# Optimization experiments

Hardware: AMD Instinct MI355X
Metric: run time of the kernel (lower is better)

## Reference

```python
import jax, jax.numpy as jnp
import numpy as np

B, K, VOC, D = 1024, 5, 32000, 128


def setup_inputs() -> dict:
    key = jax.random.key(0)
    k1, k2, k3, k4, k5 = jax.random.split(key, 5)
    return {
        "vi": jax.random.normal(k1, (B, VOC), dtype=jnp.float32),
        "vo": jax.random.normal(k2, (B, VOC), dtype=jnp.float32),
        "neg_samples": jax.random.normal(k3, (B, K, VOC), dtype=jnp.float32),
        "V": jax.random.normal(k4, (VOC, D), dtype=jnp.float32),
        "U": jax.random.normal(k5, (VOC, D), dtype=jnp.float32),
    }


def reference(vi, vo, neg_samples, V, U):
    # one-hot-style matmul embedding lookups
    vi_embed = vi @ V                                  # [B, D]
    vo_embed = vo @ U                                  # [B, D]
    # positive term: logsigmoid(<vi_embed, vo_embed>)
    left = jax.nn.log_sigmoid(jnp.sum(vi_embed * vo_embed, axis=1, keepdims=True))  # [B, 1]
    # negative samples: [B, K, D] then batched dot with vi_embed
    neg_embed = jnp.einsum("bkv,vd->bkd", neg_samples, U)   # [B, K, D]
    batch_mul = jnp.einsum("bkd,bd->bk", neg_embed, vi_embed)  # [B, K]
    right = jnp.sum(jax.nn.log_sigmoid(-batch_mul), axis=1, keepdims=True)  # [B, 1]
    return jnp.mean(-(left + right))
```

## Files before the change

### kernel.cpp

```cpp
#include <hip/hip_runtime.h>
#include <hip/hip_bf16.h>

#define B_SZ 1024
#define KNEG 5
#define VOC 32000
#define DIM 128

typedef __bf16 bf16x8 __attribute__((ext_vector_type(8)));
typedef float f32x4 __attribute__((ext_vector_type(4)));


__device__ __forceinline__ float logsig(float x) {
    return fminf(x, 0.0f) - log1pf(expf(-fabsf(x)));
}

__global__ __launch_bounds__(256) void k0_convert(
    const float* __restrict__ V, const float* __restrict__ U,
    __bf16* __restrict__ Vt, __bf16* __restrict__ Ub) {
    __shared__ float tile[32][33];
    int bid = blockIdx.x;
    int vt = bid >> 2;
    int dt = bid & 3;
    int v0 = vt * 32, d0 = dt * 32;
    int t = threadIdx.x;
    int lr = t >> 5;
    int lc = t & 31;
#pragma unroll
    for (int i = 0; i < 4; ++i) {
        int r = lr + i * 8;
        size_t idx = (size_t)(v0 + r) * DIM + d0 + lc;
        tile[r][lc] = V[idx];
        Ub[idx] = (__bf16)U[idx];
    }
    __syncthreads();
#pragma unroll
    for (int i = 0; i < 4; ++i) {
        int r = lr + i * 8;
        Vt[(size_t)(d0 + r) * VOC + v0 + lc] = (__bf16)tile[lc][r];
    }
}

__global__ __launch_bounds__(256) void k1_viembed(
    const float* __restrict__ vi, const __bf16* __restrict__ Vt,
    float* __restrict__ partial) {
    int mt = blockIdx.x;
    int sp = blockIdx.y;
    int wave = threadIdx.x >> 6;
    int lane = threadIdx.x & 63;
    int n16 = lane & 15;
    int q = lane >> 4;
    int b0 = mt * 32;

    f32x4 acc[2][8];
#pragma unroll
    for (int rt = 0; rt < 2; ++rt)
#pragma unroll
        for (int ct = 0; ct < 8; ++ct)
            acc[rt][ct] = (f32x4){0.f, 0.f, 0.f, 0.f};

    int v_base = sp * 4000;
    for (int s = wave; s < 125; s += 4) {
        int kk = v_base + s * 32 + q * 8;
        bf16x8 afrag[2];
#pragma unroll
        for (int rt = 0; rt < 2; ++rt) {
            int b = b0 + rt * 16 + n16;
            const float4* p = (const float4*)(vi + (size_t)b * VOC + kk);
            float4 x0 = p[0];
            float4 x1 = p[1];
            bf16x8 a;
            a[0] = (__bf16)x0.x; a[1] = (__bf16)x0.y;
            a[2] = (__bf16)x0.z; a[3] = (__bf16)x0.w;
            a[4] = (__bf16)x1.x; a[5] = (__bf16)x1.y;
            a[6] = (__bf16)x1.z; a[7] = (__bf16)x1.w;
            afrag[rt] = a;
        }
#pragma unroll
        for (int ct = 0; ct < 8; ++ct) {
            int d = ct * 16 + n16;
            bf16x8 bfrag = *(const bf16x8*)(Vt + (size_t)d * VOC + kk);
#pragma unroll
            for (int rt = 0; rt < 2; ++rt)
                acc[rt][ct] = __builtin_amdgcn_mfma_f32_16x16x32_bf16(
                    afrag[rt], bfrag, acc[rt][ct], 0, 0, 0);
        }
    }

    __shared__ float red[4][32][128];
#pragma unroll
    for (int rt = 0; rt < 2; ++rt)
#pragma unroll
        for (int ct = 0; ct < 8; ++ct)
#pragma unroll
            for (int r = 0; r < 4; ++r)
                red[wave][rt * 16 + q * 4 + r][ct * 16 + n16] = acc[rt][ct][r];
    __syncthreads();
    int t = threadIdx.x;
#pragma unroll
    for (int i = 0; i < 16; ++i) {
        int idx = t + i * 256;
        int bl = idx >> 7, dd = idx & 127;
        float s = red[0][bl][dd] + red[1][bl][dd] + red[2][bl][dd] + red[3][bl][dd];
        partial[((size_t)sp * B_SZ + b0 + bl) * DIM + dd] = s;
    }
}

__global__ __launch_bounds__(256) void k2_reduce(
    const float* __restrict__ partial, __bf16* __restrict__ vie) {
    int idx = blockIdx.x * 256 + threadIdx.x;
    float s = 0.f;
#pragma unroll
    for (int sp = 0; sp < 8; ++sp) s += partial[(size_t)sp * (B_SZ * DIM) + idx];
    vie[idx] = (__bf16)s;
}

__global__ __launch_bounds__(256) void k3_fused(
    const __bf16* __restrict__ vie, const float* __restrict__ vo,
    const float* __restrict__ neg, const __bf16* __restrict__ Ub,
    float* __restrict__ pos_dot, float* __restrict__ neg_dot) {
    __shared__ float W[32 * 256];
    int bt = blockIdx.x;
    int vc = blockIdx.y;
    int t = threadIdx.x;
    int wave = t >> 6, lane = t & 63, n16 = lane & 15, q = lane >> 4;
    int b0 = bt * 32;

    bf16x8 afrag[2][4];
#pragma unroll
    for (int rt = 0; rt < 2; ++rt) {
        int b = b0 + rt * 16 + n16;
#pragma unroll
        for (int ks = 0; ks < 4; ++ks)
            afrag[rt][ks] = *(const bf16x8*)(vie + (size_t)b * DIM + ks * 32 + q * 8);
    }

    int rowB = t >> 3;
    int lcol = t & 7;
    float acc[6] = {0.f, 0.f, 0.f, 0.f, 0.f, 0.f};

    int vbase = vc * 1280;
    const float* vop = vo + (size_t)(b0 + rowB) * VOC + vbase + lcol * 4;
    const float* negp[KNEG];
#pragma unroll
    for (int k = 0; k < KNEG; ++k)
        negp[k] = neg + ((size_t)(b0 + rowB) * KNEG + k) * VOC + vbase + lcol * 4;

    for (int c = 0; c < 5; ++c) {
        int vchunk = vbase + c * 256;
#pragma unroll
        for (int j = 0; j < 4; ++j) {
            int tt = wave * 4 + j;
            int v0 = vchunk + tt * 16;
            f32x4 w0 = (f32x4){0.f, 0.f, 0.f, 0.f};
            f32x4 w1 = (f32x4){0.f, 0.f, 0.f, 0.f};
#pragma unroll
            for (int ks = 0; ks < 4; ++ks) {
                bf16x8 bfrag = *(const bf16x8*)(Ub + (size_t)(v0 + n16) * DIM + ks * 32 + q * 8);
                w0 = __builtin_amdgcn_mfma_f32_16x16x32_bf16(afrag[0][ks], bfrag, w0, 0, 0, 0);
                w1 = __builtin_amdgcn_mfma_f32_16x16x32_bf16(afrag[1][ks], bfrag, w1, 0, 0, 0);
            }
            int col = tt * 16 + n16;
#pragma unroll
            for (int r = 0; r < 4; ++r) {
                W[(q * 4 + r) * 256 + col] = w0[r];
                W[(16 + q * 4 + r) * 256 + col] = w1[r];
            }
        }
        __syncthreads();
        const float* vpc = vop + c * 256;
#pragma unroll
        for (int i = 0; i < 8; ++i) {
            float4 wv = *(const float4*)&W[rowB * 256 + lcol * 4 + i * 32];
            float4 x = *(const float4*)(vpc + i * 32);
            acc[0] += x.x * wv.x + x.y * wv.y + x.z * wv.z + x.w * wv.w;
#pragma unroll
            for (int k = 0; k < KNEG; ++k) {
                float4 y = *(const float4*)(negp[k] + c * 256 + i * 32);
                acc[1 + k] += y.x * wv.x + y.y * wv.y + y.z * wv.z + y.w * wv.w;
            }
        }
        __syncthreads();
    }

#pragma unroll
    for (int j = 0; j < 6; ++j) {
        float s = acc[j];
        s += __shfl_xor(s, 1, 8);
        s += __shfl_xor(s, 2, 8);
        s += __shfl_xor(s, 4, 8);
        if (lcol == 0) {
            int b = b0 + rowB;
            if (j == 0) atomicAdd(&pos_dot[b], s);
            else atomicAdd(&neg_dot[b * KNEG + (j - 1)], s);
        }
    }
}

__global__ __launch_bounds__(256) void k4_final(
    const float* __restrict__ pos_dot, const float* __restrict__ neg_dot,
    float* __restrict__ out) {
    __shared__ float wsum[4];
    int t = threadIdx.x;
    float s = 0.f;
    for (int b = t; b < B_SZ; b += 256) {
        float left = logsig(pos_dot[b]);
        float right = 0.f;
#pragma unroll
        for (int k = 0; k < KNEG; ++k) right += logsig(-neg_dot[b * KNEG + k]);
        s += -(left + right);
    }
#pragma unroll
    for (int m = 32; m >= 1; m >>= 1) s += __shfl_xor(s, m, 64);
    if ((t & 63) == 0) wsum[t >> 6] = s;
    __syncthreads();
    if (t == 0) out[0] = (wsum[0] + wsum[1] + wsum[2] + wsum[3]) * (1.0f / B_SZ);
}

extern "C" void kernel_launch(void* const* d_in, const int* in_sizes, int n_in,
                              void* d_out, int out_size, void* d_ws, size_t ws_size,
                              hipStream_t stream) {
    const float* vi  = (const float*)d_in[0];
    const float* vo  = (const float*)d_in[1];
    const float* neg = (const float*)d_in[2];
    const float* V   = (const float*)d_in[3];
    const float* U   = (const float*)d_in[4];

    char* ws = (char*)d_ws;
    __bf16* Ub      = (__bf16*)(ws);
    __bf16* Vt      = (__bf16*)(ws + 8192000);
    float*  partial = (float*) (ws + 16384000);
    __bf16* vie     = (__bf16*)(ws + 20578304);
    float*  pos_dot = (float*) (ws + 20840448);
    float*  neg_dot = (float*) (ws + 20844544);
    float*  out     = (float*)d_out;

    hipMemsetAsync(ws + 20840448, 0, 4096 + 20480, stream);

    k0_convert<<<4000, 256, 0, stream>>>(V, U, Vt, Ub);
    k1_viembed<<<dim3(32, 8), 256, 0, stream>>>(vi, Vt, partial);
    k2_reduce<<<512, 256, 0, stream>>>(partial, vie);
    k3_fused<<<dim3(32, 25), 256, 0, stream>>>(vie, vo, neg, Ub, pos_dot, neg_dot);
    k4_final<<<1, 256, 0, stream>>>(pos_dot, neg_dot, out);
}
```

Baseline: 1.117 ms.

## Increase split-K parallelism in vi embedding and negative-sample kernels

The vi@V kernel moves from 256 blocks, each reducing over 4000 vocab entries with an in-block LDS cross-wave reduction, to 800 blocks where each wave owns 16 batch rows over a 640-wide vocab slice and writes its partial directly. The reduction kernel now sums 50 partials. The fused vo/neg kernel drops its 5-chunk loop so each block handles a single 256-wide slice, giving 4000 blocks instead of 800. The aim is more concurrent blocks to saturate memory bandwidth on the large streaming reads, at the cost of a much larger partial buffer, more atomics and repeated vie fragment loads.

```diff
diff --git a/kernel.cpp b/kernel.cpp
--- a/kernel.cpp
+++ b/kernel.cpp
@@ -5,6 +5,9 @@
 #define KNEG 5
 #define VOC 32000
 #define DIM 128
+#define NSPLIT 50
+#define VSLICE 640
+#define NS (VSLICE / 32)
 
 typedef __bf16 bf16x8 __attribute__((ext_vector_type(8)));
 typedef float f32x4 __attribute__((ext_vector_type(4)));
@@ -49,60 +52,36 @@
     int lane = threadIdx.x & 63;
     int n16 = lane & 15;
     int q = lane >> 4;
-    int b0 = mt * 32;
-
-    f32x4 acc[2][8];
-#pragma unroll
-    for (int rt = 0; rt < 2; ++rt)
-#pragma unroll
-        for (int ct = 0; ct < 8; ++ct)
-            acc[rt][ct] = (f32x4){0.f, 0.f, 0.f, 0.f};
-
-    int v_base = sp * 4000;
-    for (int s = wave; s < 125; s += 4) {
+    int brow = mt * 64 + wave * 16;
+
+    f32x4 acc[8];
+#pragma unroll
+    for (int ct = 0; ct < 8; ++ct) acc[ct] = (f32x4){0.f, 0.f, 0.f, 0.f};
+
+    int v_base = sp * VSLICE;
+    const float* arow = vi + (size_t)(brow + n16) * VOC + v_base + q * 8;
+#pragma unroll 2
+    for (int s = 0; s < NS; ++s) {
         int kk = v_base + s * 32 + q * 8;
-        bf16x8 afrag[2];
-#pragma unroll
-        for (int rt = 0; rt < 2; ++rt) {
-            int b = b0 + rt * 16 + n16;
-            const float4* p = (const float4*)(vi + (size_t)b * VOC + kk);
-            float4 x0 = p[0];
-            float4 x1 = p[1];
-            bf16x8 a;
-            a[0] = (__bf16)x0.x; a[1] = (__bf16)x0.y;
-            a[2] = (__bf16)x0.z; a[3] = (__bf16)x0.w;
-            a[4] = (__bf16)x1.x; a[5] = (__bf16)x1.y;
-            a[6] = (__bf16)x1.z; a[7] = (__bf16)x1.w;
-            afrag[rt] = a;
-        }
+        float4 x0 = *(const float4*)(arow + s * 32);
+        float4 x1 = *(const float4*)(arow + s * 32 + 4);
+        bf16x8 a;
+        a[0] = (__bf16)x0.x; a[1] = (__bf16)x0.y;
+        a[2] = (__bf16)x0.z; a[3] = (__bf16)x0.w;
+        a[4] = (__bf16)x1.x; a[5] = (__bf16)x1.y;
+        a[6] = (__bf16)x1.z; a[7] = (__bf16)x1.w;
 #pragma unroll
         for (int ct = 0; ct < 8; ++ct) {
-            int d = ct * 16 + n16;
-            bf16x8 bfrag = *(const bf16x8*)(Vt + (size_t)d * VOC + kk);
-#pragma unroll
-            for (int rt = 0; rt < 2; ++rt)
-                acc[rt][ct] = __builtin_amdgcn_mfma_f32_16x16x32_bf16(
-                    afrag[rt], bfrag, acc[rt][ct], 0, 0, 0);
-        }
-    }
-
-    __shared__ float red[4][32][128];
-#pragma unroll
-    for (int rt = 0; rt < 2; ++rt)
-#pragma unroll
-        for (int ct = 0; ct < 8; ++ct)
-#pragma unroll
-            for (int r = 0; r < 4; ++r)
-                red[wave][rt * 16 + q * 4 + r][ct * 16 + n16] = acc[rt][ct][r];
-    __syncthreads();
-    int t = threadIdx.x;
-#pragma unroll
-    for (int i = 0; i < 16; ++i) {
-        int idx = t + i * 256;
-        int bl = idx >> 7, dd = idx & 127;
-        float s = red[0][bl][dd] + red[1][bl][dd] + red[2][bl][dd] + red[3][bl][dd];
-        partial[((size_t)sp * B_SZ + b0 + bl) * DIM + dd] = s;
-    }
+            bf16x8 bfrag = *(const bf16x8*)(Vt + (size_t)(ct * 16 + n16) * VOC + kk);
+            acc[ct] = __builtin_amdgcn_mfma_f32_16x16x32_bf16(a, bfrag, acc[ct], 0, 0, 0);
+        }
+    }
+    float* pb = partial + ((size_t)sp * B_SZ + brow) * DIM;
+#pragma unroll
+    for (int ct = 0; ct < 8; ++ct)
+#pragma unroll
+        for (int r = 0; r < 4; ++r)
+            pb[(size_t)(q * 4 + r) * DIM + ct * 16 + n16] = acc[ct][r];
 }
 
 __global__ __launch_bounds__(256) void k2_reduce(
@@ -110,7 +89,7 @@
     int idx = blockIdx.x * 256 + threadIdx.x;
     float s = 0.f;
 #pragma unroll
-    for (int sp = 0; sp < 8; ++sp) s += partial[(size_t)sp * (B_SZ * DIM) + idx];
+    for (int sp = 0; sp < NSPLIT; ++sp) s += partial[(size_t)sp * (B_SZ * DIM) + idx];
     vie[idx] = (__bf16)s;
 }
 
@@ -124,6 +103,7 @@
     int t = threadIdx.x;
     int wave = t >> 6, lane = t & 63, n16 = lane & 15, q = lane >> 4;
     int b0 = bt * 32;
+    int vbase = vc * 256;
 
     bf16x8 afrag[2][4];
 #pragma unroll
@@ -133,53 +113,48 @@
         for (int ks = 0; ks < 4; ++ks)
             afrag[rt][ks] = *(const bf16x8*)(vie + (size_t)b * DIM + ks * 32 + q * 8);
     }
+
+#pragma unroll
+    for (int j = 0; j < 4; ++j) {
+        int tt = wave * 4 + j;
+        int v0 = vbase + tt * 16;
+        f32x4 w0 = (f32x4){0.f, 0.f, 0.f, 0.f};
+        f32x4 w1 = (f32x4){0.f, 0.f, 0.f, 0.f};
+#pragma unroll
+        for (int ks = 0; ks < 4; ++ks) {
+            bf16x8 bfrag = *(const bf16x8*)(Ub + (size_t)(v0 + n16) * DIM + ks * 32 + q * 8);
+            w0 = __builtin_amdgcn_mfma_f32_16x16x32_bf16(afrag[0][ks], bfrag, w0, 0, 0, 0);
+            w1 = __builtin_amdgcn_mfma_f32_16x16x32_bf16(afrag[1][ks], bfrag, w1, 0, 0, 0);
+        }
+        int col = tt * 16 + n16;
+#pragma unroll
+        for (int r = 0; r < 4; ++r) {
+            W[(q * 4 + r) * 256 + col] = w0[r];
+            W[(16 + q * 4 + r) * 256 + col] = w1[r];
+        }
+    }
+    __syncthreads();
 
     int rowB = t >> 3;
     int lcol = t & 7;
     float acc[6] = {0.f, 0.f, 0.f, 0.f, 0.f, 0.f};
 
-    int vbase = vc * 1280;
     const float* vop = vo + (size_t)(b0 + rowB) * VOC + vbase + lcol * 4;
     const float* negp[KNEG];
 #pragma unroll
     for (int k = 0; k < KNEG; ++k)
         negp[k] = neg + ((size_t)(b0 + rowB) * KNEG + k) * VOC + vbase + lcol * 4;
 
-    for (int c = 0; c < 5; ++c) {
-        int vchunk = vbase + c * 256;
-#pragma unroll
-        for (int j = 0; j < 4; ++j) {
-            int tt = wave * 4 + j;
-            int v0 = vchunk + tt * 16;
-            f32x4 w0 = (f32x4){0.f, 0.f, 0.f, 0.f};
-            f32x4 w1 = (f32x4){0.f, 0.f, 0.f, 0.f};
-#pragma unroll
-            for (int ks = 0; ks < 4; ++ks) {
-                bf16x8 bfrag = *(const bf16x8*)(Ub + (size_t)(v0 + n16) * DIM + ks * 32 + q * 8);
-                w0 = __builtin_amdgcn_mfma_f32_16x16x32_bf16(afrag[0][ks], bfrag, w0, 0, 0, 0);
-                w1 = __builtin_amdgcn_mfma_f32_16x16x32_bf16(afrag[1][ks], bfrag, w1, 0, 0, 0);
-            }
-            int col = tt * 16 + n16;
-#pragma unroll
-            for (int r = 0; r < 4; ++r) {
-                W[(q * 4 + r) * 256 + col] = w0[r];
-                W[(16 + q * 4 + r) * 256 + col] = w1[r];
-            }
-        }
-        __syncthreads();
-        const float* vpc = vop + c * 256;
-#pragma unroll
-        for (int i = 0; i < 8; ++i) {
-            float4 wv = *(const float4*)&W[rowB * 256 + lcol * 4 + i * 32];
-            float4 x = *(const float4*)(vpc + i * 32);
-            acc[0] += x.x * wv.x + x.y * wv.y + x.z * wv.z + x.w * wv.w;
-#pragma unroll
-            for (int k = 0; k < KNEG; ++k) {
-                float4 y = *(const float4*)(negp[k] + c * 256 + i * 32);
-                acc[1 + k] += y.x * wv.x + y.y * wv.y + y.z * wv.z + y.w * wv.w;
-            }
-        }
-        __syncthreads();
+#pragma unroll
+    for (int i = 0; i < 8; ++i) {
+        float4 wv = *(const float4*)&W[rowB * 256 + lcol * 4 + i * 32];
+        float4 x = *(const float4*)(vop + i * 32);
+        acc[0] += x.x * wv.x + x.y * wv.y + x.z * wv.z + x.w * wv.w;
+#pragma unroll
+        for (int k = 0; k < KNEG; ++k) {
+            float4 y = *(const float4*)(negp[k] + i * 32);
+            acc[1 + k] += y.x * wv.x + y.y * wv.y + y.z * wv.z + y.w * wv.w;
+        }
     }
 
 #pragma unroll
@@ -229,16 +204,16 @@
     __bf16* Ub      = (__bf16*)(ws);
     __bf16* Vt      = (__bf16*)(ws + 8192000);
     float*  partial = (float*) (ws + 16384000);
-    __bf16* vie     = (__bf16*)(ws + 20578304);
-    float*  pos_dot = (float*) (ws + 20840448);
-    float*  neg_dot = (float*) (ws + 20844544);
+    __bf16* vie     = (__bf16*)(ws + 42598400);
+    float*  pos_dot = (float*) (ws + 42860544);
+    float*  neg_dot = (float*) (ws + 42864640);
     float*  out     = (float*)d_out;
 
-    hipMemsetAsync(ws + 20840448, 0, 4096 + 20480, stream);
+    hipMemsetAsync(ws + 42860544, 0, 4096 + 20480, stream);
 
     k0_convert<<<4000, 256, 0, stream>>>(V, U, Vt, Ub);
-    k1_viembed<<<dim3(32, 8), 256, 0, stream>>>(vi, Vt, partial);
+    k1_viembed<<<dim3(16, 50), 256, 0, stream>>>(vi, Vt, partial);
     k2_reduce<<<512, 256, 0, stream>>>(partial, vie);
-    k3_fused<<<dim3(32, 25), 256, 0, stream>>>(vie, vo, neg, Ub, pos_dot, neg_dot);
+    k3_fused<<<dim3(32, 125), 256, 0, stream>>>(vie, vo, neg, Ub, pos_dot, neg_dot);
     k4_final<<<1, 256, 0, stream>>>(pos_dot, neg_dot, out);
 }
```

Result: faster. 1.095 ms (-2.0%).
